# Kernel tuning notes

Measured on AMD Instinct MI355X. Metric: run time of the kernel, lower is better.

## Reference

```python
import math
import jax, jax.numpy as jnp
import numpy as np

B, T, C = 8, 1024, 512
H = 8
NUM_FRAMES = 128  # num_tokens
NUM_ANIMALS = 8   # num_id; NUM_FRAMES * NUM_ANIMALS == T


def _linear_params(key, fan_in, fan_out):
    kw, kb = jax.random.split(key)
    bound = 1.0 / math.sqrt(fan_in)
    W = jax.random.uniform(kw, (fan_out, fan_in), jnp.float32, -bound, bound)
    b = jax.random.uniform(kb, (fan_out,), jnp.float32, -bound, bound)
    return W, b


def setup_inputs() -> dict:
    key = jax.random.key(0)
    ks = jax.random.split(key, 6)
    x = jax.random.normal(ks[0], (B, T, C), jnp.float32)
    mask = jnp.ones((B, T), jnp.float32)
    Wq, bq = _linear_params(ks[1], C, C)
    Wk, bk = _linear_params(ks[2], C, C)
    Wv, bv = _linear_params(ks[3], C, C)
    Wp, bp = _linear_params(ks[4], C, C)
    return {"x": x, "mask": mask, "Wq": Wq, "bq": bq, "Wk": Wk, "bk": bk,
            "Wv": Wv, "bv": bv, "Wp": Wp, "bp": bp}


def _block_causal_mask():
    # tril over frames, expanded so all animals within a frame attend to all
    # animals of frames <= current frame: kron(tril(F,F), ones(I,I)) -> (T,T)
    tril = jnp.tril(jnp.ones((NUM_FRAMES, NUM_FRAMES), jnp.float32))
    return jnp.kron(tril, jnp.ones((NUM_ANIMALS, NUM_ANIMALS), jnp.float32))


def reference(x, mask, Wq, bq, Wk, bk, Wv, bv, Wp, bp):
    Bx, Tx, Cx = x.shape
    d = Cx // H
    q = (x @ Wq.T + bq).reshape(Bx, Tx, H, d).transpose(0, 2, 1, 3)  # b h t d
    k = (x @ Wk.T + bk).reshape(Bx, Tx, H, d).transpose(0, 2, 1, 3)
    v = (x @ Wv.T + bv).reshape(Bx, Tx, H, d).transpose(0, 2, 1, 3)
    att = jnp.einsum('bhqd,bhkd->bhqk', q, k) * (1.0 / math.sqrt(d))
    m = _block_causal_mask()[None, None] * mask[:, None, None, :]  # (B,1,T,T)
    att = jnp.where(m == 0, -jnp.inf, att)
    att = jax.nn.softmax(att, axis=-1)
    # dropout is identity (pdrop=0.0 / eval mode)
    y = jnp.einsum('bhqk,bhkd->bhqd', att, v)
    y = y.transpose(0, 2, 1, 3).reshape(Bx, Tx, Cx)
    return y @ Wp.T + bp
```

## Files before the change

### kernel.cpp

```cpp
#include <hip/hip_runtime.h>
#include <cstdint>
#include <cstddef>

#define BB 8
#define TT 1024
#define CC 512
#define HH 8
#define DD 64
#define MM (BB*TT)

typedef short s16x4 __attribute__((ext_vector_type(4)));
typedef _Float16 f16x8 __attribute__((ext_vector_type(8)));
typedef _Float16 f16x2 __attribute__((ext_vector_type(2)));
typedef float f32x4  __attribute__((ext_vector_type(4)));

__device__ __forceinline__ short f2hs(float f) {
  _Float16 h = (_Float16)f;
  return __builtin_bit_cast(short, h);
}

__device__ __forceinline__ f32x4 mfma16h(f16x8 a, f16x8 b, f32x4 c) {
  return __builtin_amdgcn_mfma_f32_16x16x32_f16(a, b, c, 0, 0, 0);
}

__device__ __forceinline__ void gload_lds16(const void* g, void* l) {
  __builtin_amdgcn_global_load_lds(
      (const __attribute__((address_space(1))) unsigned int*)g,
      (__attribute__((address_space(3))) unsigned int*)l, 16, 0, 0);
}

__global__ void prep_kernel(const float* __restrict__ x,
                            const float* __restrict__ mask,
                            const float* __restrict__ Wq,
                            const float* __restrict__ Wk,
                            const float* __restrict__ Wv,
                            const float* __restrict__ Wp,
                            short* __restrict__ Xh,
                            short* __restrict__ Wqkv,
                            short* __restrict__ Wpc,
                            float* __restrict__ maskAdd) {
  const int NXv = MM * CC / 4;
  const int NWv = CC * CC / 4;
  const int NM = BB * TT;
  int stride = gridDim.x * blockDim.x;
  for (int i = blockIdx.x * blockDim.x + threadIdx.x; i < NXv + 4 * NWv + NM; i += stride) {
    if (i < NXv) {
      int e = i * 4;
      float4 v = *(const float4*)(x + e);
      s16x4 h = {f2hs(v.x), f2hs(v.y), f2hs(v.z), f2hs(v.w)};
      *(s16x4*)(Xh + e) = h;
    } else if (i < NXv + 4 * NWv) {
      int wi = i - NXv;
      int wsel = wi >> 16;
      int idx = wi & 65535;
      int r = idx >> 7, c = (idx & 127) << 2;
      const float* W = (wsel == 0) ? Wq : (wsel == 1) ? Wk : (wsel == 2) ? Wv : Wp;
      float4 v = *(const float4*)(W + (size_t)r * CC + c);
      s16x4 h = {f2hs(v.x), f2hs(v.y), f2hs(v.z), f2hs(v.w)};
      short* dst = (wsel < 3) ? (Wqkv + (size_t)(wsel * 512 + r) * CC + c)
                              : (Wpc + (size_t)r * CC + c);
      *(s16x4*)dst = h;
    } else {
      int mi = i - NXv - 4 * NWv;
      maskAdd[mi] = (mask[mi] == 0.f) ? -1e30f : 0.f;
    }
  }
}

template <int BN, int EPI>
__global__ __launch_bounds__(512, 4) void gemm_kernel(
    const short* __restrict__ A, const short* __restrict__ Bw,
    const float* __restrict__ b0, const float* __restrict__ b1,
    const float* __restrict__ b2,
    short* __restrict__ qo, short* __restrict__ ko, short* __restrict__ vt,
    float* __restrict__ outp) {
  constexpr int MR = 4;
  constexpr int NR = BN / 64;
  constexpr int ABYT = 128 * 128;
  constexpr int TILE = ABYT + BN * 128;
  constexpr int NT = 8;
  constexpr int BL = BN / 64;
  __shared__ __align__(1024) char smem[2 * TILE];

  const int tid = threadIdx.x;
  const int lane = tid & 63;
  const int w = tid >> 6;
  const int wm = w >> 2, wn = w & 3;
  const int l15 = lane & 15, lg = lane >> 4;
  const int lsw = (l15 & 7) << 4;
  const int sr8 = lane >> 3;
  const int scbsw = ((lane & 7) * 16) ^ (sr8 << 4);

  const int rowA = blockIdx.x * 128;
  const int rowB = blockIdx.y * BN;
  const char* Ab = (const char*)A + (size_t)(rowA + sr8) * 1024 + scbsw;
  const char* Bb = (const char*)Bw + (size_t)(rowB + sr8) * 1024 + scbsw;

  f32x4 acc[MR][NR] = {};

  auto STAGE_A = [&](char* dst, int kt) {
#pragma unroll
    for (int g = 0; g < 2; ++g) {
      int r0 = (w * 2 + g) * 8;
      gload_lds16(Ab + (size_t)r0 * 1024 + (size_t)kt * 128, dst + r0 * 128);
    }
  };
  auto STAGE_B = [&](char* dst, int kt) {
#pragma unroll
    for (int g = 0; g < BL; ++g) {
      int r0 = (w * BL + g) * 8;
      gload_lds16(Bb + (size_t)r0 * 1024 + (size_t)kt * 128, dst + ABYT + r0 * 128);
    }
  };
  auto RDA2 = [&](const char* buf, int mh, int kk, f16x8* af) {
#pragma unroll
    for (int i = 0; i < 2; ++i) {
      int row = wm * 64 + (mh * 2 + i) * 16 + l15;
      af[i] = *(const f16x8*)(buf + row * 128 + ((kk * 64 + lg * 16) ^ lsw));
    }
  };
  auto RDBk = [&](const char* buf, int kk, f16x8* bfr) {
#pragma unroll
    for (int j = 0; j < NR; ++j) {
      int row = wn * (BN / 4) + j * 16 + l15;
      bfr[j] = *(const f16x8*)(buf + ABYT + row * 128 + ((kk * 64 + lg * 16) ^ lsw));
    }
  };

  STAGE_A(smem, 0);
  STAGE_B(smem, 0);
  asm volatile("s_waitcnt vmcnt(0)" ::: "memory");
  __builtin_amdgcn_s_barrier();

  for (int t = 0; t < NT; ++t) {
    char* bufp = smem + (t & 1) * TILE;
    char* bufn = smem + ((t + 1) & 1) * TILE;
    f16x8 af[2], bfr[NR];

#define PH(MH)                                                                \
  __builtin_amdgcn_s_barrier();                                               \
  asm volatile("s_waitcnt lgkmcnt(0)" ::: "memory");                          \
  __builtin_amdgcn_sched_barrier(0);                                          \
  __builtin_amdgcn_s_setprio(1);                                              \
  _Pragma("unroll")                                                           \
  for (int i = 0; i < 2; ++i)                                                 \
    _Pragma("unroll")                                                         \
    for (int j = 0; j < NR; ++j)                                              \
      acc[(MH) * 2 + i][j] = mfma16h(af[i], bfr[j], acc[(MH) * 2 + i][j]);    \
  __builtin_amdgcn_s_setprio(0);

    RDBk(bufp, 0, bfr);
    RDA2(bufp, 0, 0, af);
    if (t + 1 < NT) STAGE_A(bufn, t + 1);
    PH(0)
    RDA2(bufp, 1, 0, af);
    if (t + 1 < NT) STAGE_B(bufn, t + 1);
    PH(1)
    RDBk(bufp, 1, bfr);
    RDA2(bufp, 1, 1, af);
    PH(1)
    RDA2(bufp, 0, 1, af);
    PH(0)
#undef PH
    asm volatile("s_waitcnt vmcnt(0)" ::: "memory");
    __builtin_amdgcn_s_barrier();
  }

#pragma unroll
  for (int m = 0; m < MR; ++m) {
    int rbase = rowA + wm * 64 + m * 16 + lg * 4;
#pragma unroll
    for (int n = 0; n < NR; ++n) {
      int col = rowB + wn * (BN / 4) + n * 16 + l15;
#pragma unroll
      for (int j = 0; j < 4; ++j) {
        float v = acc[m][n][j];
        int r = rbase + j;
        if constexpr (EPI == 0) {
          int b = r >> 10, t = r & 1023;
          int wsel = col >> 9, c = col & 511;
          int h = c >> 6, dd = c & 63;
          int bh = b * HH + h;
          if (wsel == 0) {
            qo[((size_t)bh * TT + t) * DD + dd] = f2hs((v + b0[c]) * 0.125f);
          } else if (wsel == 1) {
            ko[((size_t)bh * TT + t) * DD + dd] = f2hs(v + b1[c]);
          } else {
            vt[((size_t)bh * DD + dd) * TT + t] = f2hs(v + b2[c]);
          }
        } else {
          outp[(size_t)r * CC + col] = v + b0[col];
        }
      }
    }
  }
}

__global__ __launch_bounds__(512, 2) void attn_kernel(
    const short* __restrict__ q, const short* __restrict__ k,
    const short* __restrict__ vt, const float* __restrict__ maskAdd,
    short* __restrict__ Yh) {
  const int blk = blockIdx.x;
  const int p = blk & 7;
  const int bh = blk >> 3;
  const int b = bh >> 3, h = bh & 7;
  const int qbA = 8 + p;
  const int qbB = 7 - p;
  const int tid = threadIdx.x;
  const int lane = tid & 63;
  const int w = tid >> 6;
  const int wloc = w & 3;
  const int qtile = (w < 4) ? qbA : qbB;
  const int l15 = lane & 15, lg = lane >> 4;
  const int lsw = (l15 & 7) << 4;

  __shared__ short Ks[2][64 * 64];
  __shared__ short Vs[2][64 * 64];
  __shared__ short Pl[8][16 * 64];

  const short* kbh = k + (size_t)bh * TT * DD;
  const short* vbh = vt + (size_t)bh * DD * TT;

  const int srow = tid >> 3;
  const int scb = ((tid & 7) * 16) ^ ((srow & 7) << 4);

  const int qrow = qtile * 64 + wloc * 16 + l15;
  const short* qptr = q + ((size_t)bh * TT + qrow) * DD;
  f16x8 qf0 = *(const f16x8*)(qptr + lg * 8);
  f16x8 qf1 = *(const f16x8*)(qptr + 32 + lg * 8);

  f32x4 yacc[4] = {};
  float mrun = -1e30f, lrun = 0.f;

  gload_lds16((const char*)kbh + (size_t)srow * 128 + scb,
              (char*)&Ks[0][0] + srow * 128);
  gload_lds16((const char*)vbh + (size_t)srow * 2048 + scb,
              (char*)&Vs[0][0] + srow * 128);
  __syncthreads();

  int buf = 0;
  for (int jt = 0; jt <= qbA; ++jt) {
    if (jt < qbA) {
      int nt = jt + 1;
      gload_lds16((const char*)kbh + (size_t)(nt * 64 + srow) * 128 + scb,
                  (char*)&Ks[buf ^ 1][0] + srow * 128);
      gload_lds16((const char*)vbh + (size_t)srow * 2048 + nt * 128 + scb,
                  (char*)&Vs[buf ^ 1][0] + srow * 128);
    }
    if (jt <= qtile) {
      f32x4 sacc[4];
#pragma unroll
      for (int n = 0; n < 4; ++n)
        sacc[n] = *(const f32x4*)(maskAdd + (size_t)b * TT + jt * 64 + n * 16 + lg * 4);
      __builtin_amdgcn_s_setprio(1);
#pragma unroll
      for (int c = 0; c < 2; ++c) {
        f16x8 qc = (c == 0) ? qf0 : qf1;
#pragma unroll
        for (int n = 0; n < 4; ++n) {
          int krow = n * 16 + l15;
          const f16x8 kf = *(const f16x8*)((const char*)&Ks[buf][0] + krow * 128 + ((c * 64 + lg * 16) ^ lsw));
          sacc[n] = mfma16h(kf, qc, sacc[n]);
        }
      }
      __builtin_amdgcn_s_setprio(0);
      if (jt == qtile) {
        const int qloc8 = (wloc * 16 + l15) >> 3;
#pragma unroll
        for (int n = 0; n < 4; ++n)
#pragma unroll
          for (int jj = 0; jj < 4; ++jj) {
            int kloc = n * 16 + lg * 4 + jj;
            if ((kloc >> 3) > qloc8) sacc[n][jj] = -1e30f;
          }
      }
      float t0 = fmaxf(fmaxf(sacc[0][0], sacc[0][1]), fmaxf(sacc[0][2], sacc[0][3]));
      float t1 = fmaxf(fmaxf(sacc[1][0], sacc[1][1]), fmaxf(sacc[1][2], sacc[1][3]));
      float t2 = fmaxf(fmaxf(sacc[2][0], sacc[2][1]), fmaxf(sacc[2][2], sacc[2][3]));
      float t3 = fmaxf(fmaxf(sacc[3][0], sacc[3][1]), fmaxf(sacc[3][2], sacc[3][3]));
      float pmL = fmaxf(fmaxf(t0, t1), fmaxf(t2, t3));
      if (!__all(pmL <= mrun + 8.0f)) {
        float pm = fmaxf(pmL, __shfl_xor(pmL, 16));
        pm = fmaxf(pm, __shfl_xor(pm, 32));
        float mnew = fmaxf(mrun, pm);
        float alpha = __expf(mrun - mnew);
        mrun = mnew;
        lrun *= alpha;
        float ab[4];
#pragma unroll
        for (int jj = 0; jj < 4; ++jj) ab[jj] = __shfl(alpha, lg * 4 + jj);
#pragma unroll
        for (int dt = 0; dt < 4; ++dt)
#pragma unroll
          for (int jj = 0; jj < 4; ++jj) yacc[dt][jj] *= ab[jj];
      }
      float psum = 0.f;
#pragma unroll
      for (int n = 0; n < 4; ++n) {
        float p0 = __expf(sacc[n][0] - mrun);
        float p1 = __expf(sacc[n][1] - mrun);
        float p2 = __expf(sacc[n][2] - mrun);
        float p3 = __expf(sacc[n][3] - mrun);
        psum += (p0 + p1) + (p2 + p3);
        uint2 pw;
        pw.x = __builtin_bit_cast(unsigned, __builtin_amdgcn_cvt_pkrtz(p0, p1));
        pw.y = __builtin_bit_cast(unsigned, __builtin_amdgcn_cvt_pkrtz(p2, p3));
        *(uint2*)((char*)&Pl[w][0] + l15 * 128 + ((n * 32 + lg * 8) ^ lsw)) = pw;
      }
      psum += __shfl_xor(psum, 16);
      psum += __shfl_xor(psum, 32);
      lrun += psum;
      __builtin_amdgcn_s_setprio(1);
#pragma unroll
      for (int c = 0; c < 2; ++c) {
        const f16x8 pa = *(const f16x8*)((const char*)&Pl[w][0] + l15 * 128 + ((c * 64 + lg * 16) ^ lsw));
#pragma unroll
        for (int dt = 0; dt < 4; ++dt) {
          int vrow = dt * 16 + l15;
          const f16x8 vf = *(const f16x8*)((const char*)&Vs[buf][0] + vrow * 128 + ((c * 64 + lg * 16) ^ lsw));
          yacc[dt] = mfma16h(pa, vf, yacc[dt]);
        }
      }
      __builtin_amdgcn_s_setprio(0);
    }
    __syncthreads();
    buf ^= 1;
  }

  float lb[4];
#pragma unroll
  for (int jj = 0; jj < 4; ++jj) lb[jj] = 1.f / __shfl(lrun, lg * 4 + jj);
#pragma unroll
  for (int dt = 0; dt < 4; ++dt) {
    int col = h * DD + dt * 16 + l15;
#pragma unroll
    for (int jj = 0; jj < 4; ++jj) {
      int row = b * TT + qtile * 64 + wloc * 16 + lg * 4 + jj;
      float y = yacc[dt][jj] * lb[jj];
      Yh[(size_t)row * CC + col] = f2hs(y);
    }
  }
}

extern "C" void kernel_launch(void* const* d_in, const int* in_sizes, int n_in,
                              void* d_out, int out_size, void* d_ws, size_t ws_size,
                              hipStream_t stream) {
  const float* x    = (const float*)d_in[0];
  const float* mask = (const float*)d_in[1];
  const float* Wq   = (const float*)d_in[2];
  const float* bq   = (const float*)d_in[3];
  const float* Wk   = (const float*)d_in[4];
  const float* bk   = (const float*)d_in[5];
  const float* Wv   = (const float*)d_in[6];
  const float* bv   = (const float*)d_in[7];
  const float* Wp   = (const float*)d_in[8];
  const float* bp   = (const float*)d_in[9];
  float* out = (float*)d_out;

  char* ws = (char*)d_ws;
  short* Xh   = (short*)(ws);
  short* Wqkv = (short*)(ws + (size_t)8 * 1048576);
  short* Wpc  = (short*)(ws + (size_t)10 * 1048576);
  short* qo   = (short*)(ws + (size_t)11 * 1048576);
  short* ko   = (short*)(ws + (size_t)19 * 1048576);
  short* vt   = (short*)(ws + (size_t)27 * 1048576);
  short* Yh   = (short*)(ws + (size_t)35 * 1048576);
  float* maskAdd = (float*)(ws + (size_t)43 * 1048576);

  prep_kernel<<<2048, 256, 0, stream>>>(x, mask, Wq, Wk, Wv, Wp, Xh, Wqkv, Wpc, maskAdd);

  gemm_kernel<192, 0><<<dim3(64, 8), 512, 0, stream>>>(
      Xh, Wqkv, bq, bk, bv, qo, ko, vt, nullptr);

  attn_kernel<<<dim3(512), 512, 0, stream>>>(qo, ko, vt, maskAdd, Yh);

  gemm_kernel<128, 1><<<dim3(64, 4), 512, 0, stream>>>(
      Yh, Wpc, bp, nullptr, nullptr, nullptr, nullptr, nullptr, out);
}
```

Measured before the change: 74.11 us.

## Triple-buffer K/V tiles in attention with partial vmcnt waits

Moves the attention kernel's K/V staging from double to triple buffering, prefetching two tiles ahead with global_load_lds. The full __syncthreads is replaced by explicit s_waitcnt vmcnt(2) plus s_barrier, so the next tile's loads can stay in flight across the barrier. Mask loads are issued before the prefetch. The intent is to hide more global-load latency. The cost is more LDS per block, which could limit occupancy at two blocks per CU, and the correctness of the counted waits relies on the in-order vmcnt accounting.

```diff
diff --git a/kernel.cpp b/kernel.cpp
--- a/kernel.cpp
+++ b/kernel.cpp
@@ -11,7 +11,6 @@
 
 typedef short s16x4 __attribute__((ext_vector_type(4)));
 typedef _Float16 f16x8 __attribute__((ext_vector_type(8)));
-typedef _Float16 f16x2 __attribute__((ext_vector_type(2)));
 typedef float f32x4  __attribute__((ext_vector_type(4)));
 
 __device__ __forceinline__ short f2hs(float f) {
@@ -214,8 +213,8 @@
   const int l15 = lane & 15, lg = lane >> 4;
   const int lsw = (l15 & 7) << 4;
 
-  __shared__ short Ks[2][64 * 64];
-  __shared__ short Vs[2][64 * 64];
+  __shared__ short Ks[3][64 * 64];
+  __shared__ short Vs[3][64 * 64];
   __shared__ short Pl[8][16 * 64];
 
   const short* kbh = k + (size_t)bh * TT * DD;
@@ -223,6 +222,13 @@
 
   const int srow = tid >> 3;
   const int scb = ((tid & 7) * 16) ^ ((srow & 7) << 4);
+
+  auto STAGE = [&](int bs, int tile) {
+    gload_lds16((const char*)kbh + ((size_t)tile * 64 + srow) * 128 + scb,
+                (char*)&Ks[bs][0] + srow * 128);
+    gload_lds16((const char*)vbh + (size_t)srow * 2048 + tile * 128 + scb,
+                (char*)&Vs[bs][0] + srow * 128);
+  };
 
   const int qrow = qtile * 64 + wloc * 16 + l15;
   const short* qptr = q + ((size_t)bh * TT + qrow) * DD;
@@ -232,26 +238,27 @@
   f32x4 yacc[4] = {};
   float mrun = -1e30f, lrun = 0.f;
 
-  gload_lds16((const char*)kbh + (size_t)srow * 128 + scb,
-              (char*)&Ks[0][0] + srow * 128);
-  gload_lds16((const char*)vbh + (size_t)srow * 2048 + scb,
-              (char*)&Vs[0][0] + srow * 128);
-  __syncthreads();
-
-  int buf = 0;
+  STAGE(0, 0);
+  STAGE(1, 1);
+  asm volatile("s_waitcnt vmcnt(2) lgkmcnt(0)" ::: "memory");
+  __builtin_amdgcn_s_barrier();
+
   for (int jt = 0; jt <= qbA; ++jt) {
-    if (jt < qbA) {
-      int nt = jt + 1;
-      gload_lds16((const char*)kbh + (size_t)(nt * 64 + srow) * 128 + scb,
-                  (char*)&Ks[buf ^ 1][0] + srow * 128);
-      gload_lds16((const char*)vbh + (size_t)srow * 2048 + nt * 128 + scb,
-                  (char*)&Vs[buf ^ 1][0] + srow * 128);
-    }
-    if (jt <= qtile) {
+    const int cb = jt % 3;
+    const bool act = (jt <= qtile);
+    f32x4 mav[4];
+    if (act) {
+#pragma unroll
+      for (int n = 0; n < 4; ++n)
+        mav[n] = *(const f32x4*)(maskAdd + (size_t)b * TT + jt * 64 + n * 16 + lg * 4);
+    }
+    const bool staged = (jt + 2 <= qbA);
+    if (staged) STAGE((jt + 2) % 3, jt + 2);
+
+    if (act) {
       f32x4 sacc[4];
 #pragma unroll
-      for (int n = 0; n < 4; ++n)
-        sacc[n] = *(const f32x4*)(maskAdd + (size_t)b * TT + jt * 64 + n * 16 + lg * 4);
+      for (int n = 0; n < 4; ++n) sacc[n] = mav[n];
       __builtin_amdgcn_s_setprio(1);
 #pragma unroll
       for (int c = 0; c < 2; ++c) {
@@ -259,7 +266,7 @@
 #pragma unroll
         for (int n = 0; n < 4; ++n) {
           int krow = n * 16 + l15;
-          const f16x8 kf = *(const f16x8*)((const char*)&Ks[buf][0] + krow * 128 + ((c * 64 + lg * 16) ^ lsw));
+          const f16x8 kf = *(const f16x8*)((const char*)&Ks[cb][0] + krow * 128 + ((c * 64 + lg * 16) ^ lsw));
           sacc[n] = mfma16h(kf, qc, sacc[n]);
         }
       }
@@ -317,14 +324,18 @@
 #pragma unroll
         for (int dt = 0; dt < 4; ++dt) {
           int vrow = dt * 16 + l15;
-          const f16x8 vf = *(const f16x8*)((const char*)&Vs[buf][0] + vrow * 128 + ((c * 64 + lg * 16) ^ lsw));
+          const f16x8 vf = *(const f16x8*)((const char*)&Vs[cb][0] + vrow * 128 + ((c * 64 + lg * 16) ^ lsw));
           yacc[dt] = mfma16h(pa, vf, yacc[dt]);
         }
       }
       __builtin_amdgcn_s_setprio(0);
     }
-    __syncthreads();
-    buf ^= 1;
+    if (staged) {
+      asm volatile("s_waitcnt vmcnt(2) lgkmcnt(0)" ::: "memory");
+    } else {
+      asm volatile("s_waitcnt vmcnt(0) lgkmcnt(0)" ::: "memory");
+    }
+    __builtin_amdgcn_s_barrier();
   }
 
   float lb[4];
```

Result: no change. 74.84 us (+1.0%).

## Split attention into one-tile blocks with register-shuffled P and longest-first ordering

Applied to the files above, without the earlier changes.

The attention kernel changes from 512-thread blocks that pair two complementary query tiles to 256-thread blocks that each handle a single query tile, launched as 1024 blocks. Block indices are arranged so the tiles with the most causal work are scheduled first. The P matrix is now rearranged into the MFMA A-operand layout with cross-lane shuffles instead of a round trip through LDS, which drops the Pl buffer. In exchange, the K/V tiles are staged by more blocks and wave occupancy per block changes; the shuffle sequence adds ALU work.

```diff
diff --git a/kernel.cpp b/kernel.cpp
--- a/kernel.cpp
+++ b/kernel.cpp
@@ -11,8 +11,8 @@
 
 typedef short s16x4 __attribute__((ext_vector_type(4)));
 typedef _Float16 f16x8 __attribute__((ext_vector_type(8)));
-typedef _Float16 f16x2 __attribute__((ext_vector_type(2)));
 typedef float f32x4  __attribute__((ext_vector_type(4)));
+typedef unsigned u32x4 __attribute__((ext_vector_type(4)));
 
 __device__ __forceinline__ short f2hs(float f) {
   _Float16 h = (_Float16)f;
@@ -196,146 +196,165 @@
   }
 }
 
-__global__ __launch_bounds__(512, 2) void attn_kernel(
+__global__ __launch_bounds__(256, 4) void attn_kernel(
     const short* __restrict__ q, const short* __restrict__ k,
     const short* __restrict__ vt, const float* __restrict__ maskAdd,
     short* __restrict__ Yh) {
   const int blk = blockIdx.x;
-  const int p = blk & 7;
-  const int bh = blk >> 3;
+  const int k4 = blk >> 8;
+  const int r = blk & 255;
+  const int bh = r >> 2;
+  const int j4 = r & 3;
+  const int qb = (k4 & 1) ? ((k4 & 2) ? (4 + j4) : j4)
+                          : ((k4 & 2) ? (11 - j4) : (15 - j4));
   const int b = bh >> 3, h = bh & 7;
-  const int qbA = 8 + p;
-  const int qbB = 7 - p;
   const int tid = threadIdx.x;
   const int lane = tid & 63;
   const int w = tid >> 6;
-  const int wloc = w & 3;
-  const int qtile = (w < 4) ? qbA : qbB;
   const int l15 = lane & 15, lg = lane >> 4;
   const int lsw = (l15 & 7) << 4;
 
   __shared__ short Ks[2][64 * 64];
   __shared__ short Vs[2][64 * 64];
-  __shared__ short Pl[8][16 * 64];
 
   const short* kbh = k + (size_t)bh * TT * DD;
   const short* vbh = vt + (size_t)bh * DD * TT;
 
-  const int srow = tid >> 3;
-  const int scb = ((tid & 7) * 16) ^ ((srow & 7) << 4);
-
-  const int qrow = qtile * 64 + wloc * 16 + l15;
+  const int sr32 = tid >> 3;
+  const int scb = (tid & 7) * 16;
+
+  auto STAGE = [&](int bs, int tile) {
+#pragma unroll
+    for (int g = 0; g < 2; ++g) {
+      int row = g * 32 + sr32;
+      int sw = (row & 7) << 4;
+      gload_lds16((const char*)kbh + ((size_t)tile * 64 + row) * 128 + (scb ^ sw),
+                  (char*)&Ks[bs][0] + row * 128);
+      gload_lds16((const char*)vbh + (size_t)row * 2048 + tile * 128 + (scb ^ sw),
+                  (char*)&Vs[bs][0] + row * 128);
+    }
+  };
+
+  const int qrow = qb * 64 + w * 16 + l15;
   const short* qptr = q + ((size_t)bh * TT + qrow) * DD;
   f16x8 qf0 = *(const f16x8*)(qptr + lg * 8);
   f16x8 qf1 = *(const f16x8*)(qptr + 32 + lg * 8);
 
   f32x4 yacc[4] = {};
-  float mrun = -1e30f, lrun = 0.f;
-
-  gload_lds16((const char*)kbh + (size_t)srow * 128 + scb,
-              (char*)&Ks[0][0] + srow * 128);
-  gload_lds16((const char*)vbh + (size_t)srow * 2048 + scb,
-              (char*)&Vs[0][0] + srow * 128);
+  float mrun = -1e30f, lpart = 0.f;
+
+  const int srcA = (((2 * lg) & 3) << 4) + l15;
+  const int srcB = (((2 * lg + 1) & 3) << 4) + l15;
+  const bool hiSel = (lg >= 2);
+
+  STAGE(0, 0);
   __syncthreads();
 
   int buf = 0;
-  for (int jt = 0; jt <= qbA; ++jt) {
-    if (jt < qbA) {
-      int nt = jt + 1;
-      gload_lds16((const char*)kbh + (size_t)(nt * 64 + srow) * 128 + scb,
-                  (char*)&Ks[buf ^ 1][0] + srow * 128);
-      gload_lds16((const char*)vbh + (size_t)srow * 2048 + nt * 128 + scb,
-                  (char*)&Vs[buf ^ 1][0] + srow * 128);
-    }
-    if (jt <= qtile) {
-      f32x4 sacc[4];
+  for (int jt = 0; jt <= qb; ++jt) {
+    if (jt < qb) STAGE(buf ^ 1, jt + 1);
+
+    f32x4 sacc[4];
+#pragma unroll
+    for (int n = 0; n < 4; ++n)
+      sacc[n] = *(const f32x4*)(maskAdd + (size_t)b * TT + jt * 64 + n * 16 + lg * 4);
+    __builtin_amdgcn_s_setprio(1);
+#pragma unroll
+    for (int c = 0; c < 2; ++c) {
+      f16x8 qc = (c == 0) ? qf0 : qf1;
+#pragma unroll
+      for (int n = 0; n < 4; ++n) {
+        int krow = n * 16 + l15;
+        const f16x8 kf = *(const f16x8*)((const char*)&Ks[buf][0] + krow * 128 + ((c * 64 + lg * 16) ^ lsw));
+        sacc[n] = mfma16h(kf, qc, sacc[n]);
+      }
+    }
+    __builtin_amdgcn_s_setprio(0);
+    if (jt == qb) {
+      const int qloc8 = (w * 16 + l15) >> 3;
 #pragma unroll
       for (int n = 0; n < 4; ++n)
-        sacc[n] = *(const f32x4*)(maskAdd + (size_t)b * TT + jt * 64 + n * 16 + lg * 4);
-      __builtin_amdgcn_s_setprio(1);
-#pragma unroll
-      for (int c = 0; c < 2; ++c) {
-        f16x8 qc = (c == 0) ? qf0 : qf1;
-#pragma unroll
-        for (int n = 0; n < 4; ++n) {
-          int krow = n * 16 + l15;
-          const f16x8 kf = *(const f16x8*)((const char*)&Ks[buf][0] + krow * 128 + ((c * 64 + lg * 16) ^ lsw));
-          sacc[n] = mfma16h(kf, qc, sacc[n]);
+#pragma unroll
+        for (int jj = 0; jj < 4; ++jj) {
+          int kloc = n * 16 + lg * 4 + jj;
+          if ((kloc >> 3) > qloc8) sacc[n][jj] = -1e30f;
         }
+    }
+    float t0 = fmaxf(fmaxf(sacc[0][0], sacc[0][1]), fmaxf(sacc[0][2], sacc[0][3]));
+    float t1 = fmaxf(fmaxf(sacc[1][0], sacc[1][1]), fmaxf(sacc[1][2], sacc[1][3]));
+    float t2 = fmaxf(fmaxf(sacc[2][0], sacc[2][1]), fmaxf(sacc[2][2], sacc[2][3]));
+    float t3 = fmaxf(fmaxf(sacc[3][0], sacc[3][1]), fmaxf(sacc[3][2], sacc[3][3]));
+    float pmL = fmaxf(fmaxf(t0, t1), fmaxf(t2, t3));
+    if (!__all(pmL <= mrun + 8.0f)) {
+      float pm = fmaxf(pmL, __shfl_xor(pmL, 16));
+      pm = fmaxf(pm, __shfl_xor(pm, 32));
+      float mnew = fmaxf(mrun, pm);
+      float alpha = __expf(mrun - mnew);
+      mrun = mnew;
+      lpart *= alpha;
+      float ab[4];
+#pragma unroll
+      for (int jj = 0; jj < 4; ++jj) ab[jj] = __shfl(alpha, lg * 4 + jj);
+#pragma unroll
+      for (int dt = 0; dt < 4; ++dt)
+#pragma unroll
+        for (int jj = 0; jj < 4; ++jj) yacc[dt][jj] *= ab[jj];
+    }
+    unsigned pk2[4][2];
+    float lps = 0.f;
+#pragma unroll
+    for (int n = 0; n < 4; ++n) {
+      float p0 = __expf(sacc[n][0] - mrun);
+      float p1 = __expf(sacc[n][1] - mrun);
+      float p2 = __expf(sacc[n][2] - mrun);
+      float p3 = __expf(sacc[n][3] - mrun);
+      lps += (p0 + p1) + (p2 + p3);
+      pk2[n][0] = __builtin_bit_cast(unsigned, __builtin_amdgcn_cvt_pkrtz(p0, p1));
+      pk2[n][1] = __builtin_bit_cast(unsigned, __builtin_amdgcn_cvt_pkrtz(p2, p3));
+    }
+    lpart += lps;
+    f16x8 pa[2];
+#pragma unroll
+    for (int c = 0; c < 2; ++c) {
+      unsigned a0 = __shfl(pk2[2 * c][0], srcA);
+      unsigned a1 = __shfl(pk2[2 * c][1], srcA);
+      unsigned a2 = __shfl(pk2[2 * c][0], srcB);
+      unsigned a3 = __shfl(pk2[2 * c][1], srcB);
+      unsigned b0 = __shfl(pk2[2 * c + 1][0], srcA);
+      unsigned b1 = __shfl(pk2[2 * c + 1][1], srcA);
+      unsigned b2 = __shfl(pk2[2 * c + 1][0], srcB);
+      unsigned b3 = __shfl(pk2[2 * c + 1][1], srcB);
+      u32x4 tv = {hiSel ? b0 : a0, hiSel ? b1 : a1, hiSel ? b2 : a2, hiSel ? b3 : a3};
+      pa[c] = __builtin_bit_cast(f16x8, tv);
+    }
+    __builtin_amdgcn_s_setprio(1);
+#pragma unroll
+    for (int c = 0; c < 2; ++c) {
+#pragma unroll
+      for (int dt = 0; dt < 4; ++dt) {
+        int vrow = dt * 16 + l15;
+        const f16x8 vf = *(const f16x8*)((const char*)&Vs[buf][0] + vrow * 128 + ((c * 64 + lg * 16) ^ lsw));
+        yacc[dt] = mfma16h(pa[c], vf, yacc[dt]);
       }
-      __builtin_amdgcn_s_setprio(0);
-      if (jt == qtile) {
-        const int qloc8 = (wloc * 16 + l15) >> 3;
-#pragma unroll
-        for (int n = 0; n < 4; ++n)
-#pragma unroll
-          for (int jj = 0; jj < 4; ++jj) {
-            int kloc = n * 16 + lg * 4 + jj;
-            if ((kloc >> 3) > qloc8) sacc[n][jj] = -1e30f;
-          }
-      }
-      float t0 = fmaxf(fmaxf(sacc[0][0], sacc[0][1]), fmaxf(sacc[0][2], sacc[0][3]));
-      float t1 = fmaxf(fmaxf(sacc[1][0], sacc[1][1]), fmaxf(sacc[1][2], sacc[1][3]));
-      float t2 = fmaxf(fmaxf(sacc[2][0], sacc[2][1]), fmaxf(sacc[2][2], sacc[2][3]));
-      float t3 = fmaxf(fmaxf(sacc[3][0], sacc[3][1]), fmaxf(sacc[3][2], sacc[3][3]));
-      float pmL = fmaxf(fmaxf(t0, t1), fmaxf(t2, t3));
-      if (!__all(pmL <= mrun + 8.0f)) {
-        float pm = fmaxf(pmL, __shfl_xor(pmL, 16));
-        pm = fmaxf(pm, __shfl_xor(pm, 32));
-        float mnew = fmaxf(mrun, pm);
-        float alpha = __expf(mrun - mnew);
-        mrun = mnew;
-        lrun *= alpha;
-        float ab[4];
-#pragma unroll
-        for (int jj = 0; jj < 4; ++jj) ab[jj] = __shfl(alpha, lg * 4 + jj);
-#pragma unroll
-        for (int dt = 0; dt < 4; ++dt)
-#pragma unroll
-          for (int jj = 0; jj < 4; ++jj) yacc[dt][jj] *= ab[jj];
-      }
-      float psum = 0.f;
-#pragma unroll
-      for (int n = 0; n < 4; ++n) {
-        float p0 = __expf(sacc[n][0] - mrun);
-        float p1 = __expf(sacc[n][1] - mrun);
-        float p2 = __expf(sacc[n][2] - mrun);
-        float p3 = __expf(sacc[n][3] - mrun);
-        psum += (p0 + p1) + (p2 + p3);
-        uint2 pw;
-        pw.x = __builtin_bit_cast(unsigned, __builtin_amdgcn_cvt_pkrtz(p0, p1));
-        pw.y = __builtin_bit_cast(unsigned, __builtin_amdgcn_cvt_pkrtz(p2, p3));
-        *(uint2*)((char*)&Pl[w][0] + l15 * 128 + ((n * 32 + lg * 8) ^ lsw)) = pw;
-      }
-      psum += __shfl_xor(psum, 16);
-      psum += __shfl_xor(psum, 32);
-      lrun += psum;
-      __builtin_amdgcn_s_setprio(1);
-#pragma unroll
-      for (int c = 0; c < 2; ++c) {
-        const f16x8 pa = *(const f16x8*)((const char*)&Pl[w][0] + l15 * 128 + ((c * 64 + lg * 16) ^ lsw));
-#pragma unroll
-        for (int dt = 0; dt < 4; ++dt) {
-          int vrow = dt * 16 + l15;
-          const f16x8 vf = *(const f16x8*)((const char*)&Vs[buf][0] + vrow * 128 + ((c * 64 + lg * 16) ^ lsw));
-          yacc[dt] = mfma16h(pa, vf, yacc[dt]);
-        }
-      }
-      __builtin_amdgcn_s_setprio(0);
-    }
+    }
+    __builtin_amdgcn_s_setprio(0);
+
     __syncthreads();
     buf ^= 1;
   }
 
+  float lr = lpart;
+  lr += __shfl_xor(lr, 16);
+  lr += __shfl_xor(lr, 32);
   float lb[4];
 #pragma unroll
-  for (int jj = 0; jj < 4; ++jj) lb[jj] = 1.f / __shfl(lrun, lg * 4 + jj);
+  for (int jj = 0; jj < 4; ++jj) lb[jj] = 1.f / __shfl(lr, lg * 4 + jj);
 #pragma unroll
   for (int dt = 0; dt < 4; ++dt) {
     int col = h * DD + dt * 16 + l15;
 #pragma unroll
     for (int jj = 0; jj < 4; ++jj) {
-      int row = b * TT + qtile * 64 + wloc * 16 + lg * 4 + jj;
+      int row = b * TT + qb * 64 + w * 16 + lg * 4 + jj;
       float y = yacc[dt][jj] * lb[jj];
       Yh[(size_t)row * CC + col] = f2hs(y);
     }
@@ -372,7 +391,7 @@
   gemm_kernel<192, 0><<<dim3(64, 8), 512, 0, stream>>>(
       Xh, Wqkv, bq, bk, bv, qo, ko, vt, nullptr);
 
-  attn_kernel<<<dim3(512), 512, 0, stream>>>(qo, ko, vt, maskAdd, Yh);
+  attn_kernel<<<dim3(1024), 256, 0, stream>>>(qo, ko, vt, maskAdd, Yh);
 
   gemm_kernel<128, 1><<<dim3(64, 4), 512, 0, stream>>>(
       Yh, Wpc, bp, nullptr, nullptr, nullptr, nullptr, nullptr, out);
```

New measurement: 73.33 us. No clear change (-1.1%).
